# Performance work log

Measured on AMD Instinct MI355X. Metric: run time of the kernel, lower is better.

The kernel has to match this reference:

```python
import jax, jax.numpy as jnp
import numpy as np

PE_DIM = 40  # pe_dim; gaussian PE scale factor = pe_dim // 2


def _batched_linear(x, wb):
    # x: [B, N, D], wb: [B, D+1, H] (last row is bias)
    return jnp.einsum('bnd,bdh->bnh', x, wb[:, :-1, :]) + wb[:, -1:, :]


def setup_inputs() -> dict:
    key = jax.random.key(0)
    ks = jax.random.split(key, 8)
    B, N = 16, 16384
    H = 256
    pe_out = 3 * PE_DIM  # 120
    s = 0.05  # keep ReLU-chain activations bounded
    return {
        'x': jax.random.normal(ks[0], (B, N, 3), dtype=jnp.float32),
        'wb0': jax.random.normal(ks[1], (B, pe_out + 1, H), dtype=jnp.float32) * s,
        'wb1': jax.random.normal(ks[2], (B, H + 1, H), dtype=jnp.float32) * s,
        'wb2': jax.random.normal(ks[3], (B, H + 1, H), dtype=jnp.float32) * s,
        'wb3': jax.random.normal(ks[4], (B, H + 1, H), dtype=jnp.float32) * s,
        'wb4': jax.random.normal(ks[5], (B, H + 1, H), dtype=jnp.float32) * s,
        'wb_out': jax.random.normal(ks[6], (B, H + 1, 1), dtype=jnp.float32) * s,
        'rand_freqs': jax.random.normal(ks[7], (3 * (PE_DIM // 2), 3), dtype=jnp.float32),  # feat_sigma=1
    }


def reference(x, wb0, wb1, wb2, wb3, wb4, wb_out, rand_freqs):
    # Gaussian positional encoding: k = x . (rand_freqs * pe_dim//2)
    k = jnp.einsum('bnd,fd->bnf', x, rand_freqs * (PE_DIM // 2))  # [B,N,60]
    h = jnp.concatenate([jnp.sin(k), jnp.cos(k)], axis=-1)        # [B,N,120]
    for wb in (wb0, wb1, wb2, wb3, wb4):
        h = jax.nn.relu(_batched_linear(h, wb))
    out = _batched_linear(h, wb_out)  # [B,N,1]
    return out
```

## Files before the change

### kernel.cpp

```cpp
#include <hip/hip_runtime.h>
#include <hip/hip_bf16.h>


#define H 256
#define MT 128
#define HP 264
#define PE_NF 60

typedef __attribute__((ext_vector_type(8))) short s16x8;
typedef __attribute__((ext_vector_type(4))) float f32x4;

static __device__ __forceinline__ unsigned short f2bf(float v) {
  unsigned int u = __float_as_uint(v);
  return (unsigned short)((u + 0x7FFFu + ((u >> 16) & 1u)) >> 16);
}
static __device__ __forceinline__ float bf2f(unsigned short u) {
  return __uint_as_float(((unsigned int)u) << 16);
}

__global__ __launch_bounds__(256) void prep_weights(
    const float* __restrict__ wb0, const float* __restrict__ wb1,
    const float* __restrict__ wb2, const float* __restrict__ wb3,
    const float* __restrict__ wb4,
    unsigned short* __restrict__ w0t, unsigned short* __restrict__ w14t,
    float* __restrict__ biases) {
  int z = blockIdx.z;
  int li = z >> 4, b = z & 15;
  int k0 = blockIdx.x * 32;
  int n0 = blockIdx.y * 32;
  int Ks, Kd;
  const float* src;
  unsigned short* dst;
  if (li == 0) {
    Ks = 120; Kd = 128;
    if (k0 >= 128) return;
    src = wb0 + (size_t)b * 121 * H;
    dst = w0t + (size_t)b * H * 128;
  } else {
    Ks = 256; Kd = 256;
    const float* srcs[4] = {wb1, wb2, wb3, wb4};
    src = srcs[li - 1] + (size_t)b * 257 * H;
    dst = w14t + ((size_t)(li - 1) * 16 + b) * H * 256;
  }
  __shared__ float tile[32][33];
  int tx = threadIdx.x & 31, ty0 = threadIdx.x >> 5;
#pragma unroll
  for (int i = 0; i < 4; ++i) {
    int k = k0 + ty0 + i * 8;
    tile[ty0 + i * 8][tx] = (k < Ks) ? src[(size_t)k * H + n0 + tx] : 0.f;
  }
  if (k0 == 0 && ty0 == 0)
    biases[((size_t)li * 16 + b) * H + n0 + tx] = src[(size_t)Ks * H + n0 + tx];
  __syncthreads();
#pragma unroll
  for (int i = 0; i < 4; ++i) {
    int n = n0 + ty0 + i * 8;
    dst[(size_t)n * Kd + k0 + tx] = f2bf(tile[tx][ty0 + i * 8]);
  }
}

__global__ __launch_bounds__(256, 2) void hyponerf_main(
    const float* __restrict__ x, const float* __restrict__ rfreq,
    const float* __restrict__ wbout,
    const unsigned short* __restrict__ w0t, const unsigned short* __restrict__ w14t,
    const float* __restrict__ biases, float* __restrict__ out) {
  __shared__ __align__(16) unsigned short h_s[MT * HP];
  __shared__ float fr_s[PE_NF * 3];
  __shared__ float x_s[MT * 3];
  __shared__ float wout_s[H + 1];

  int bid = blockIdx.x;
  int logical = (bid & 7) * 256 + (bid >> 3);
  int b  = logical >> 7;
  int mt = logical & 127;

  int t = threadIdx.x;
  int w = t >> 6, l = t & 63;
  int rlane = l & 15;
  int kgrp  = l >> 4;
  int klane = kgrp * 8;
  int colb  = w * 64 + rlane;

  const float* xg = x + ((size_t)b * 16384 + (size_t)mt * MT) * 3;
  for (int i = t; i < MT * 3; i += 256) x_s[i] = xg[i];
  for (int i = t; i < PE_NF * 3; i += 256) fr_s[i] = rfreq[i] * 20.0f;
  for (int i = t; i < H + 1; i += 256) wout_s[i] = wbout[(size_t)b * (H + 1) + i];
  __syncthreads();

  {
    int r = t >> 1;
    int fb = (t & 1) * 30;
    float x0 = x_s[r * 3 + 0], x1 = x_s[r * 3 + 1], x2 = x_s[r * 3 + 2];
#pragma unroll
    for (int j = 0; j < 30; ++j) {
      int f = fb + j;
      float kv = x0 * fr_s[f * 3 + 0] + x1 * fr_s[f * 3 + 1] + x2 * fr_s[f * 3 + 2];
      float sv, cv;
      __sincosf(kv, &sv, &cv);
      h_s[r * HP + f]      = f2bf(sv);
      h_s[r * HP + 60 + f] = f2bf(cv);
    }
    if ((t & 1) == 0) {
#pragma unroll
      for (int p = 120; p < 128; ++p) h_s[r * HP + p] = 0;
    }
  }
  __syncthreads();

#pragma unroll 1
  for (int li = 0; li < 5; ++li) {
    const int K = (li == 0) ? 128 : 256;
    const unsigned short* wl = (li == 0)
        ? (w0t + (size_t)b * H * 128)
        : (w14t + ((size_t)(li - 1) * 16 + b) * H * 256);
    const float* bl = biases + ((size_t)li * 16 + b) * H;

    f32x4 acc[8][4];
#pragma unroll
    for (int rt = 0; rt < 8; ++rt)
#pragma unroll
      for (int ct = 0; ct < 4; ++ct)
        acc[rt][ct] = (f32x4){0.f, 0.f, 0.f, 0.f};

    int aoff[8];
#pragma unroll
    for (int rt = 0; rt < 8; ++rt) aoff[rt] = (rt * 16 + rlane) * HP + klane;
    const unsigned short* wp[4];
#pragma unroll
    for (int ct = 0; ct < 4; ++ct)
      wp[ct] = wl + (size_t)(colb + ct * 16) * K + klane;

    const int nkt = K >> 5;
#pragma unroll 1
    for (int kt = 0; kt < nkt; ++kt) {
      s16x8 bfr[4], afr[8];
#pragma unroll
      for (int ct = 0; ct < 4; ++ct) {
        bfr[ct] = *(const s16x8*)wp[ct];
        wp[ct] += 32;
      }
#pragma unroll
      for (int rt = 0; rt < 8; ++rt)
        afr[rt] = *(const s16x8*)&h_s[aoff[rt] + kt * 32];
#pragma unroll
      for (int rt = 0; rt < 8; ++rt)
#pragma unroll
        for (int ct = 0; ct < 4; ++ct)
          acc[rt][ct] = __builtin_amdgcn_mfma_f32_16x16x32_bf16(
              afr[rt], bfr[ct], acc[rt][ct], 0, 0, 0);
    }
    __syncthreads();

    float bc[4];
#pragma unroll
    for (int ct = 0; ct < 4; ++ct) bc[ct] = bl[colb + ct * 16];
#pragma unroll
    for (int rt = 0; rt < 8; ++rt)
#pragma unroll
      for (int ct = 0; ct < 4; ++ct)
#pragma unroll
        for (int g = 0; g < 4; ++g) {
          float v = acc[rt][ct][g] + bc[ct];
          v = fmaxf(v, 0.f);
          h_s[(rt * 16 + kgrp * 4 + g) * HP + colb + ct * 16] = f2bf(v);
        }
    __syncthreads();
  }

  {
    int r = t >> 1;
    int kb = (t & 1) * 128;
    float sum = 0.f;
#pragma unroll
    for (int c = 0; c < 16; ++c) {
      int kc = kb + ((c + r) & 15) * 8;
      const s16x8 hv = *(const s16x8*)&h_s[r * HP + kc];
#pragma unroll
      for (int j = 0; j < 8; ++j)
        sum += bf2f((unsigned short)hv[j]) * wout_s[kc + j];
    }
    sum += __shfl_xor(sum, 1);
    if ((t & 1) == 0)
      out[(size_t)b * 16384 + (size_t)mt * MT + r] = sum + wout_s[H];
  }
}

extern "C" void kernel_launch(void* const* d_in, const int* in_sizes, int n_in,
                              void* d_out, int out_size, void* d_ws, size_t ws_size,
                              hipStream_t stream) {
  const float* x     = (const float*)d_in[0];
  const float* wb0   = (const float*)d_in[1];
  const float* wb1   = (const float*)d_in[2];
  const float* wb2   = (const float*)d_in[3];
  const float* wb3   = (const float*)d_in[4];
  const float* wb4   = (const float*)d_in[5];
  const float* wbout = (const float*)d_in[6];
  const float* rfreq = (const float*)d_in[7];
  float* out = (float*)d_out;

  char* ws = (char*)d_ws;
  unsigned short* w0t  = (unsigned short*)ws;
  unsigned short* w14t = (unsigned short*)(ws + (size_t)16 * 256 * 128 * 2);
  float* biases = (float*)(ws + (size_t)16 * 256 * 128 * 2
                              + (size_t)4 * 16 * 256 * 256 * 2);

  prep_weights<<<dim3(8, 8, 80), 256, 0, stream>>>(wb0, wb1, wb2, wb3, wb4,
                                                   w0t, w14t, biases);
  hyponerf_main<<<dim3(2048), 256, 0, stream>>>(x, rfreq, wbout, w0t, w14t,
                                                biases, out);
}
```

Measured before the change: 199.1 us.

## Swizzle activation LDS layout, transpose MFMA operands, prefetch weights, fold bias into accumulators

Replaces the padded activation LDS layout with an XOR-swizzled unpadded layout and swaps the MFMA operand order so each lane holds four consecutive output columns. Epilogue stores can then be packed into 8-byte bf16x4 writes instead of scalar 2-byte stores. Weight fragments for the next k-step are double-buffered in registers with a fully unrolled, templated k-loop. Bias is preloaded into the accumulators. The aim is fewer LDS bank conflicts and store instructions and better hiding of global load latency, at the cost of more registers, which could hurt occupancy at 2 waves per SIMD.

New measurement: 193.8 us. 1.03x faster.

```diff
diff --git a/kernel.cpp b/kernel.cpp
--- a/kernel.cpp
+++ b/kernel.cpp
@@ -4,7 +4,6 @@
 
 #define H 256
 #define MT 128
-#define HP 264
 #define PE_NF 60
 
 typedef __attribute__((ext_vector_type(8))) short s16x8;
@@ -16,6 +15,9 @@
 }
 static __device__ __forceinline__ float bf2f(unsigned short u) {
   return __uint_as_float(((unsigned int)u) << 16);
+}
+static __device__ __forceinline__ int hswz(int row, int chunk) {
+  return (chunk & ~7) | ((chunk ^ row) & 7);
 }
 
 __global__ __launch_bounds__(256) void prep_weights(
@@ -59,12 +61,86 @@
   }
 }
 
+template <int NKT>
+static __device__ __forceinline__ void mlp_layer(
+    const unsigned short* __restrict__ wl, const float* __restrict__ bl,
+    unsigned short* __restrict__ h_s, const int rlane, const int kgrp,
+    const int w) {
+  const int n_base = w * 64;
+
+  f32x4 acc[8][4];
+  {
+    f32x4 bini[4];
+#pragma unroll
+    for (int ct = 0; ct < 4; ++ct)
+      bini[ct] = *(const f32x4*)(bl + n_base + ct * 16 + kgrp * 4);
+#pragma unroll
+    for (int rt = 0; rt < 8; ++rt)
+#pragma unroll
+      for (int ct = 0; ct < 4; ++ct) acc[rt][ct] = bini[ct];
+  }
+
+  const unsigned short* wp[4];
+#pragma unroll
+  for (int ct = 0; ct < 4; ++ct)
+    wp[ct] = wl + (size_t)(n_base + ct * 16 + rlane) * (NKT * 32) + kgrp * 8;
+  int aoff[8];
+#pragma unroll
+  for (int rt = 0; rt < 8; ++rt) aoff[rt] = (rt * 16 + rlane) * 256;
+
+  s16x8 bb[2][4];
+#pragma unroll
+  for (int ct = 0; ct < 4; ++ct) bb[0][ct] = *(const s16x8*)(wp[ct]);
+
+#pragma unroll
+  for (int kt = 0; kt < NKT; ++kt) {
+    if (kt + 1 < NKT) {
+#pragma unroll
+      for (int ct = 0; ct < 4; ++ct)
+        bb[(kt + 1) & 1][ct] = *(const s16x8*)(wp[ct] + (kt + 1) * 32);
+    }
+    s16x8 afr[8];
+    const int cs = hswz(rlane, kt * 4 + kgrp) * 8;
+#pragma unroll
+    for (int rt = 0; rt < 8; ++rt)
+      afr[rt] = *(const s16x8*)&h_s[aoff[rt] + cs];
+#pragma unroll
+    for (int rt = 0; rt < 8; ++rt)
+#pragma unroll
+      for (int ct = 0; ct < 4; ++ct)
+        acc[rt][ct] = __builtin_amdgcn_mfma_f32_16x16x32_bf16(
+            bb[kt & 1][ct], afr[rt], acc[rt][ct], 0, 0, 0);
+  }
+  __syncthreads();
+
+  const int sub = (kgrp & 1) * 4;
+  const int cbase = w * 8 + (kgrp >> 1);
+#pragma unroll
+  for (int rt = 0; rt < 8; ++rt) {
+    const int m = rt * 16 + rlane;
+    const int rowb = m * 256;
+#pragma unroll
+    for (int ct = 0; ct < 4; ++ct) {
+      const int cs = hswz(m, cbase + ct * 2);
+      float v0 = fmaxf(acc[rt][ct][0], 0.f);
+      float v1 = fmaxf(acc[rt][ct][1], 0.f);
+      float v2 = fmaxf(acc[rt][ct][2], 0.f);
+      float v3 = fmaxf(acc[rt][ct][3], 0.f);
+      union { __hip_bfloat162 h2[2]; uint2 u; } pk;
+      pk.h2[0] = __float22bfloat162_rn(float2{v0, v1});
+      pk.h2[1] = __float22bfloat162_rn(float2{v2, v3});
+      *(uint2*)&h_s[rowb + cs * 8 + sub] = pk.u;
+    }
+  }
+  __syncthreads();
+}
+
 __global__ __launch_bounds__(256, 2) void hyponerf_main(
     const float* __restrict__ x, const float* __restrict__ rfreq,
     const float* __restrict__ wbout,
     const unsigned short* __restrict__ w0t, const unsigned short* __restrict__ w14t,
     const float* __restrict__ biases, float* __restrict__ out) {
-  __shared__ __align__(16) unsigned short h_s[MT * HP];
+  __shared__ __align__(16) unsigned short h_s[MT * 256];
   __shared__ float fr_s[PE_NF * 3];
   __shared__ float x_s[MT * 3];
   __shared__ float wout_s[H + 1];
@@ -78,8 +154,6 @@
   int w = t >> 6, l = t & 63;
   int rlane = l & 15;
   int kgrp  = l >> 4;
-  int klane = kgrp * 8;
-  int colb  = w * 64 + rlane;
 
   const float* xg = x + ((size_t)b * 16384 + (size_t)mt * MT) * 3;
   for (int i = t; i < MT * 3; i += 256) x_s[i] = xg[i];
@@ -91,93 +165,45 @@
     int r = t >> 1;
     int fb = (t & 1) * 30;
     float x0 = x_s[r * 3 + 0], x1 = x_s[r * 3 + 1], x2 = x_s[r * 3 + 2];
+    int rowb = r * 256;
 #pragma unroll
     for (int j = 0; j < 30; ++j) {
       int f = fb + j;
       float kv = x0 * fr_s[f * 3 + 0] + x1 * fr_s[f * 3 + 1] + x2 * fr_s[f * 3 + 2];
       float sv, cv;
       __sincosf(kv, &sv, &cv);
-      h_s[r * HP + f]      = f2bf(sv);
-      h_s[r * HP + 60 + f] = f2bf(cv);
+      h_s[rowb + hswz(r, f >> 3) * 8 + (f & 7)] = f2bf(sv);
+      int g = 60 + f;
+      h_s[rowb + hswz(r, g >> 3) * 8 + (g & 7)] = f2bf(cv);
     }
     if ((t & 1) == 0) {
-#pragma unroll
-      for (int p = 120; p < 128; ++p) h_s[r * HP + p] = 0;
-    }
-  }
-  __syncthreads();
-
+      int cs = hswz(r, 15) * 8;
+#pragma unroll
+      for (int p = 0; p < 8; ++p) h_s[rowb + cs + p] = 0;
+    }
+  }
+  __syncthreads();
+
+  mlp_layer<4>(w0t + (size_t)b * H * 128, biases + (size_t)b * H, h_s,
+               rlane, kgrp, w);
 #pragma unroll 1
-  for (int li = 0; li < 5; ++li) {
-    const int K = (li == 0) ? 128 : 256;
-    const unsigned short* wl = (li == 0)
-        ? (w0t + (size_t)b * H * 128)
-        : (w14t + ((size_t)(li - 1) * 16 + b) * H * 256);
-    const float* bl = biases + ((size_t)li * 16 + b) * H;
-
-    f32x4 acc[8][4];
-#pragma unroll
-    for (int rt = 0; rt < 8; ++rt)
-#pragma unroll
-      for (int ct = 0; ct < 4; ++ct)
-        acc[rt][ct] = (f32x4){0.f, 0.f, 0.f, 0.f};
-
-    int aoff[8];
-#pragma unroll
-    for (int rt = 0; rt < 8; ++rt) aoff[rt] = (rt * 16 + rlane) * HP + klane;
-    const unsigned short* wp[4];
-#pragma unroll
-    for (int ct = 0; ct < 4; ++ct)
-      wp[ct] = wl + (size_t)(colb + ct * 16) * K + klane;
-
-    const int nkt = K >> 5;
-#pragma unroll 1
-    for (int kt = 0; kt < nkt; ++kt) {
-      s16x8 bfr[4], afr[8];
-#pragma unroll
-      for (int ct = 0; ct < 4; ++ct) {
-        bfr[ct] = *(const s16x8*)wp[ct];
-        wp[ct] += 32;
-      }
-#pragma unroll
-      for (int rt = 0; rt < 8; ++rt)
-        afr[rt] = *(const s16x8*)&h_s[aoff[rt] + kt * 32];
-#pragma unroll
-      for (int rt = 0; rt < 8; ++rt)
-#pragma unroll
-        for (int ct = 0; ct < 4; ++ct)
-          acc[rt][ct] = __builtin_amdgcn_mfma_f32_16x16x32_bf16(
-              afr[rt], bfr[ct], acc[rt][ct], 0, 0, 0);
-    }
-    __syncthreads();
-
-    float bc[4];
-#pragma unroll
-    for (int ct = 0; ct < 4; ++ct) bc[ct] = bl[colb + ct * 16];
-#pragma unroll
-    for (int rt = 0; rt < 8; ++rt)
-#pragma unroll
-      for (int ct = 0; ct < 4; ++ct)
-#pragma unroll
-        for (int g = 0; g < 4; ++g) {
-          float v = acc[rt][ct][g] + bc[ct];
-          v = fmaxf(v, 0.f);
-          h_s[(rt * 16 + kgrp * 4 + g) * HP + colb + ct * 16] = f2bf(v);
-        }
-    __syncthreads();
+  for (int li = 1; li < 5; ++li) {
+    mlp_layer<8>(w14t + ((size_t)(li - 1) * 16 + b) * H * 256,
+                 biases + ((size_t)li * 16 + b) * H, h_s, rlane, kgrp, w);
   }
 
   {
     int r = t >> 1;
-    int kb = (t & 1) * 128;
+    int cb = (t & 1) * 16;
+    int rowb = r * 256;
     float sum = 0.f;
 #pragma unroll
     for (int c = 0; c < 16; ++c) {
-      int kc = kb + ((c + r) & 15) * 8;
-      const s16x8 hv = *(const s16x8*)&h_s[r * HP + kc];
+      int ch = cb + c;
+      const s16x8 hv = *(const s16x8*)&h_s[rowb + hswz(r, ch) * 8];
 #pragma unroll
       for (int j = 0; j < 8; ++j)
-        sum += bf2f((unsigned short)hv[j]) * wout_s[kc + j];
+        sum += bf2f((unsigned short)hv[j]) * wout_s[ch * 8 + j];
     }
     sum += __shfl_xor(sum, 1);
     if ((t & 1) == 0)
```
